# Kernel tuning notes

Hardware: AMD Instinct MI355X
Metric: run time of the kernel (lower is better)

The kernel has to match this reference:

```python
import jax, jax.numpy as jnp
import numpy as np

B, S, D, E, K = 4, 2048, 1024, 8, 2
H = 4 * D


def setup_inputs() -> dict:
    key = jax.random.key(0)
    k0, k1, k2, k3 = jax.random.split(key, 4)
    x = jax.random.normal(k0, (B, S, D), dtype=jnp.float32)
    router_w = jax.random.normal(k1, (E, D), dtype=jnp.float32) * 0.02
    w1 = jax.random.normal(k2, (E, H, D), dtype=jnp.float32) * 0.02  # fc1 weight [out,in]
    w2 = jax.random.normal(k3, (E, D, H), dtype=jnp.float32) * 0.02  # fc2 weight [out,in]
    return {"x": x, "router_w": router_w, "w1": w1, "w2": w2}


def reference(x, router_w, w1, w2):
    b, s, d = x.shape
    e = router_w.shape[0]
    # Router: logits = x @ router_w.T (nn.Linear, bias=False)
    logits = jnp.einsum('bsd,ed->bse', x, router_w)
    probs = jax.nn.softmax(logits, axis=-1)
    topk_vals, topk_idx = jax.lax.top_k(probs, K)  # [b,s,K]

    x_flat = x.reshape(b * s, d)                  # [T, D]
    vals = topk_vals.reshape(b * s, K)            # [T, K]
    idx = topk_idx.reshape(b * s, K)              # [T, K]

    out = jnp.zeros_like(x_flat)
    # Small fixed loop over experts (8); each token gets summed routing weight
    # for this expert over its K slots (equivalent to the torch per-slot scatter-add).
    for eid in range(e):
        w = jnp.sum(jnp.where(idx == eid, vals, jnp.zeros((), x.dtype)), axis=-1)  # [T]
        h = jax.nn.gelu(x_flat @ w1[eid].T, approximate=False)  # [T, H], exact GELU like F.gelu
        y = h @ w2[eid].T                                        # [T, D]
        out = out + w[:, None] * y
    return out.reshape(b, s, d)
```

## Files before the change

kernel.cpp:

```cpp
#include <hip/hip_runtime.h>
#include <hip/hip_bf16.h>
#include <cstdint>

#define TN 8192
#define DN 1024
#define HN 4096
#define EN 8
#define PADMAX 18432

typedef __attribute__((ext_vector_type(8))) short short8;
typedef __attribute__((ext_vector_type(4))) float f32x4;
typedef __attribute__((ext_vector_type(4))) unsigned short ushort4v;

__device__ inline unsigned short f2bf(float f) {
  unsigned u = __builtin_bit_cast(unsigned, f);
  u = u + 0x7fffu + ((u >> 16) & 1u);
  return (unsigned short)(u >> 16);
}
__device__ inline float bf2f(unsigned short u) {
  unsigned v = ((unsigned)u) << 16;
  return __builtin_bit_cast(float, v);
}

__device__ inline float gelu_f(float v) {
  float z2 = 1.5957691216057308f * (v + 0.044715f * v * v * v);
  return v / (1.f + __expf(-z2));
}

__device__ inline void gload_lds16(const void* g, void* l) {
  __builtin_amdgcn_global_load_lds(
      (const __attribute__((address_space(1))) unsigned int*)g,
      (__attribute__((address_space(3))) unsigned int*)l, 16, 0, 0);
}

__global__ __launch_bounds__(256) void cvtw_k(const float* __restrict__ w1,
                                              const float* __restrict__ w2,
                                              unsigned short* __restrict__ d1,
                                              unsigned short* __restrict__ d2) {
  long g = ((long)blockIdx.x * 256 + threadIdx.x) * 8;
  const float* s = blockIdx.y ? w2 : w1;
  unsigned short* d = blockIdx.y ? d2 : d1;
  float4 v0 = *(const float4*)(s + g);
  float4 v1 = *(const float4*)(s + g + 4);
  short8 pk;
  pk[0] = (short)f2bf(v0.x); pk[1] = (short)f2bf(v0.y);
  pk[2] = (short)f2bf(v0.z); pk[3] = (short)f2bf(v0.w);
  pk[4] = (short)f2bf(v1.x); pk[5] = (short)f2bf(v1.y);
  pk[6] = (short)f2bf(v1.z); pk[7] = (short)f2bf(v1.w);
  *(short8*)(d + g) = pk;
}

__global__ __launch_bounds__(256) void router_k(const float* __restrict__ x,
                                                const float* __restrict__ rw,
                                                int* __restrict__ eids,
                                                float* __restrict__ wts) {
  int wid = threadIdx.x >> 6, lane = threadIdx.x & 63;
  int t = blockIdx.x * 4 + wid;
  const float* xr = x + (long)t * DN;
  float a[EN];
#pragma unroll
  for (int e = 0; e < EN; ++e) a[e] = 0.f;
  for (int k = lane; k < DN; k += 64) {
    float xv = xr[k];
#pragma unroll
    for (int e = 0; e < EN; ++e) a[e] += xv * rw[e * DN + k];
  }
#pragma unroll
  for (int off = 32; off > 0; off >>= 1) {
#pragma unroll
    for (int e = 0; e < EN; ++e) a[e] += __shfl_xor(a[e], off);
  }
  if (lane == 0) {
    float mx = a[0];
#pragma unroll
    for (int e = 1; e < EN; ++e) mx = fmaxf(mx, a[e]);
    float p[EN], s = 0.f;
#pragma unroll
    for (int e = 0; e < EN; ++e) { p[e] = __expf(a[e] - mx); s += p[e]; }
    int e0 = 0; float b0 = p[0];
#pragma unroll
    for (int e = 1; e < EN; ++e) if (p[e] > b0) { b0 = p[e]; e0 = e; }
    int e1 = -1; float b1 = -1.f;
#pragma unroll
    for (int e = 0; e < EN; ++e) if (e != e0 && p[e] > b1) { b1 = p[e]; e1 = e; }
    float inv = 1.f / s;
    eids[2 * t] = e0; eids[2 * t + 1] = e1;
    wts[2 * t] = b0 * inv; wts[2 * t + 1] = b1 * inv;
  }
}

__global__ __launch_bounds__(1024) void count_k(const int* __restrict__ eids,
                                                int* __restrict__ poff) {
  __shared__ int hist[16][EN];
  int tid = threadIdx.x, lane = tid & 63, w = tid >> 6;
  int c[EN];
#pragma unroll
  for (int e = 0; e < EN; ++e) c[e] = 0;
  for (int i = tid; i < 2 * TN; i += 1024) {
    int e = eids[i];
#pragma unroll
    for (int j = 0; j < EN; ++j) c[j] += (e == j) ? 1 : 0;
  }
#pragma unroll
  for (int j = 0; j < EN; ++j) {
#pragma unroll
    for (int off = 32; off > 0; off >>= 1) c[j] += __shfl_xor(c[j], off);
  }
  if (lane == 0) {
#pragma unroll
    for (int j = 0; j < EN; ++j) hist[w][j] = c[j];
  }
  __syncthreads();
  if (tid == 0) {
    int o = 0;
    for (int e = 0; e < EN; ++e) {
      int s = 0;
      for (int ww = 0; ww < 16; ++ww) s += hist[ww][e];
      poff[e] = o;
      o += (s + 127) & ~127;
    }
    poff[EN] = o;
  }
}

__global__ __launch_bounds__(256) void scatter_k(const int* __restrict__ eids,
                                                 const float* __restrict__ wts,
                                                 const int* __restrict__ poff,
                                                 int* __restrict__ cursor,
                                                 int* __restrict__ pairTok,
                                                 float* __restrict__ pairW,
                                                 int* __restrict__ slotPos) {
  int t = blockIdx.x * 256 + threadIdx.x;
#pragma unroll
  for (int k = 0; k < 2; ++k) {
    int e = eids[2 * t + k];
    int p = atomicAdd(&cursor[e], 1);
    int pos = poff[e] + p;
    pairTok[pos] = t;
    pairW[pos] = wts[2 * t + k];
    slotPos[2 * t + k] = pos;
  }
}

__global__ __launch_bounds__(256) void gather_k(const float* __restrict__ x,
                                                const int* __restrict__ pairTok,
                                                unsigned short* __restrict__ xg) {
  int p = blockIdx.x * 4 + (threadIdx.x >> 6);
  int lane = threadIdx.x & 63;
  int tok = pairTok[p];
  if (tok < 0) tok = 0;
  const float4* src = (const float4*)(x + (long)tok * DN);
  short8* dst = (short8*)(xg + (long)p * DN);
#pragma unroll
  for (int half = 0; half < 2; ++half) {
    int e8 = half * 64 + lane;
    float4 v0 = src[e8 * 2];
    float4 v1 = src[e8 * 2 + 1];
    short8 pk;
    pk[0] = (short)f2bf(v0.x); pk[1] = (short)f2bf(v0.y);
    pk[2] = (short)f2bf(v0.z); pk[3] = (short)f2bf(v0.w);
    pk[4] = (short)f2bf(v1.x); pk[5] = (short)f2bf(v1.y);
    pk[6] = (short)f2bf(v1.z); pk[7] = (short)f2bf(v1.w);
    dst[e8] = pk;
  }
}

__global__ __launch_bounds__(256) void combine_k(const unsigned short* __restrict__ yb,
                                                 const float* __restrict__ wts,
                                                 const int* __restrict__ slotPos,
                                                 float* __restrict__ out) {
  int t = blockIdx.x;
  int p0 = slotPos[2 * t], p1 = slotPos[2 * t + 1];
  float w0 = wts[2 * t], w1 = wts[2 * t + 1];
  int c = threadIdx.x * 4;
  ushort4v y0 = *(const ushort4v*)(yb + (long)p0 * DN + c);
  ushort4v y1 = *(const ushort4v*)(yb + (long)p1 * DN + c);
  float4 o;
  o.x = w0 * bf2f(y0.x) + w1 * bf2f(y1.x);
  o.y = w0 * bf2f(y0.y) + w1 * bf2f(y1.y);
  o.z = w0 * bf2f(y0.z) + w1 * bf2f(y1.z);
  o.w = w0 * bf2f(y0.w) + w1 * bf2f(y1.w);
  *(float4*)(out + (long)t * DN + c) = o;
}


#define BAR() { asm volatile("" ::: "memory"); __builtin_amdgcn_s_barrier(); \
                asm volatile("" ::: "memory"); }
#define LGKM0() { asm volatile("s_waitcnt lgkmcnt(0)" ::: "memory"); }

#define LDA4(PAR) { const char* _b = smem + (PAR)*16384;                             \
  _Pragma("unroll") for (int m = 0; m < 4; ++m) {                                    \
    int row = waveM*64 + m*16 + (lane & 15); int cb = row * 128;                     \
    a[m][0] = *(const short8*)(_b + cb + (((lane>>4) ^ (row&7)) * 16));              \
    a[m][1] = *(const short8*)(_b + cb + (((4 + (lane>>4)) ^ (row&7)) * 16)); } }

#define LDB2(NH, PAR) { const char* _b = smem + 32768 + (PAR)*16384;                 \
  _Pragma("unroll") for (int n = 0; n < 2; ++n) {                                    \
    int row = waveN*64 + ((NH)*2+n)*16 + (lane & 15); int cb = row * 128;            \
    b[(NH)*2+n][0] = *(const short8*)(_b + cb + (((lane>>4) ^ (row&7)) * 16));       \
    b[(NH)*2+n][1] = *(const short8*)(_b + cb + (((4 + (lane>>4)) ^ (row&7)) * 16)); } }

#define MM16(NH) { __builtin_amdgcn_s_setprio(1);                                    \
  _Pragma("unroll") for (int m = 0; m < 4; ++m)                                      \
    _Pragma("unroll") for (int n = 0; n < 2; ++n) {                                  \
      acc[m][(NH)*2+n] = __builtin_amdgcn_mfma_f32_16x16x32_bf16(                    \
          a[m][0], b[(NH)*2+n][0], acc[m][(NH)*2+n], 0, 0, 0);                       \
      acc[m][(NH)*2+n] = __builtin_amdgcn_mfma_f32_16x16x32_bf16(                    \
          a[m][1], b[(NH)*2+n][1], acc[m][(NH)*2+n], 0, 0, 0); }                     \
  __builtin_amdgcn_s_setprio(0); }

template <int MODE, bool BBF16>
__global__ __launch_bounds__(256, 2) void moe_gemm128_k(
    const unsigned short* __restrict__ Ab, const void* __restrict__ Bsrc,
    void* __restrict__ OutP, const int* __restrict__ pairTok,
    const float* __restrict__ pairW, const int* __restrict__ poff, int chunkStart) {
  constexpr int KD = (MODE == 1) ? DN : HN;
  constexpr int ND = (MODE == 1) ? HN : DN;
  constexpr int SPLIT = (MODE == 3) ? 2 : 1;
  constexpr int KLEN = KD / SPLIT;
  constexpr int NT = KLEN / 64;

  extern __shared__ char smem[];

  int NX = gridDim.x;
  int NXY = NX * gridDim.y;
  int orig = blockIdx.y * NX + blockIdx.x;
  int qq = NXY >> 3, rrm = NXY & 7;
  int xcd = orig & 7, pos = orig >> 3;
  int wg = (xcd < rrm ? xcd * (qq + 1) : rrm * (qq + 1) + (xcd - rrm) * qq) + pos;

  int NYt = NXY / NX;
  const int GH = 8;
  int npg = GH * NX;
  int gid = wg / npg;
  int rem = wg - gid * npg;
  int rowsLeft = NYt - gid * GH;
  int gh = rowsLeft < GH ? rowsLeft : GH;
  int row = gid * GH + rem % gh;
  int col = rem / gh;
  int tileN = col * 128;
  int tileStart = chunkStart + row * 128;

  int Ppad = poff[EN];
  if (tileStart >= Ppad) return;
  int e = 0;
  while (e < EN - 1 && tileStart >= poff[e + 1]) ++e;

  int tid = threadIdx.x;
  int wid = tid >> 6, lane = tid & 63;
  int waveM = wid >> 1, waveN = wid & 1;
  int kbase = (MODE == 3) ? blockIdx.z * KLEN : 0;

  int r0 = tid >> 3;
  const char* aSrc[4];
  const char* bSrc[4];
#pragma unroll
  for (int j = 0; j < 4; ++j) {
    int rw_ = j * 32 + r0;
    int s = (tid & 7) ^ (rw_ & 7);
    long abase = (MODE == 1) ? (long)(tileStart + rw_) * KD
                             : (long)(tileStart - chunkStart + rw_) * KD;
    aSrc[j] = (const char*)(Ab + abase + kbase + s * 8);
    long bb = (long)e * ND * KD + (long)(tileN + rw_) * KD + kbase + s * 8;
    bSrc[j] = (const char*)Bsrc + bb * (BBF16 ? 2 : 4);
  }

  auto stageA = [&](int k0, int par) {
#pragma unroll
    for (int j = 0; j < 4; ++j)
      gload_lds16(aSrc[j] + (long)k0 * 2, smem + par * 16384 + (j * 256 + tid) * 16);
  };
  auto stageB = [&](int k0, int par) {
    if constexpr (BBF16) {
#pragma unroll
      for (int j = 0; j < 4; ++j)
        gload_lds16(bSrc[j] + (long)k0 * 2, smem + 32768 + par * 16384 + (j * 256 + tid) * 16);
    } else {
#pragma unroll
      for (int j = 0; j < 4; ++j) {
        const float4* pf = (const float4*)(bSrc[j] + (long)k0 * 4);
        float4 v0 = pf[0], v1 = pf[1];
        short8 pk;
        pk[0] = (short)f2bf(v0.x); pk[1] = (short)f2bf(v0.y);
        pk[2] = (short)f2bf(v0.z); pk[3] = (short)f2bf(v0.w);
        pk[4] = (short)f2bf(v1.x); pk[5] = (short)f2bf(v1.y);
        pk[6] = (short)f2bf(v1.z); pk[7] = (short)f2bf(v1.w);
        *(short8*)(smem + 32768 + par * 16384 + (j * 256 + tid) * 16) = pk;
      }
    }
  };

  f32x4 acc[4][4];
#pragma unroll
  for (int m = 0; m < 4; ++m)
#pragma unroll
    for (int n = 0; n < 4; ++n) acc[m][n] = (f32x4){0.f, 0.f, 0.f, 0.f};
  short8 a[4][2], b[4][2];

  stageA(0, 0); stageB(0, 0);
  stageA(64, 1); stageB(64, 1);
  if constexpr (BBF16) {
    asm volatile("s_waitcnt vmcnt(8)" ::: "memory");
  } else {
    asm volatile("s_waitcnt vmcnt(0) lgkmcnt(0)" ::: "memory");
  }
  BAR();

  for (int t = 0; t < NT; ++t) {
    int P = t & 1;
    int k2 = (t + 2) * 64;
    LDA4(P); LDB2(0, P);
    BAR(); LGKM0();
    MM16(0);
    BAR();
    LDB2(1, P);
    if (t + 2 < NT) stageA(k2, P);
    BAR(); LGKM0();
    MM16(1);
    if (t + 2 < NT) stageB(k2, P);
    if (BBF16 && t + 2 < NT) {
      asm volatile("s_waitcnt vmcnt(8)" ::: "memory");
    } else {
      asm volatile("s_waitcnt vmcnt(0)" ::: "memory");
    }
    BAR();
  }

  if (MODE == 1) {
    unsigned short* hbp = (unsigned short*)OutP;
    int rl0 = tileStart - chunkStart + waveM * 64;
#pragma unroll
    for (int m = 0; m < 4; ++m) {
#pragma unroll
      for (int r = 0; r < 4; ++r) {
        int rl = rl0 + m * 16 + (lane >> 4) * 4 + r;
#pragma unroll
        for (int n = 0; n < 4; ++n) {
          int coln = tileN + waveN * 64 + n * 16 + (lane & 15);
          hbp[(long)rl * HN + coln] = f2bf(gelu_f(acc[m][n][r]));
        }
      }
    }
  } else if (MODE == 2) {
    unsigned short* ybp = (unsigned short*)OutP;
#pragma unroll
    for (int m = 0; m < 4; ++m) {
#pragma unroll
      for (int r = 0; r < 4; ++r) {
        int p = tileStart + waveM * 64 + m * 16 + (lane >> 4) * 4 + r;
#pragma unroll
        for (int n = 0; n < 4; ++n) {
          int coln = tileN + waveN * 64 + n * 16 + (lane & 15);
          ybp[(long)p * ND + coln] = f2bf(acc[m][n][r]);
        }
      }
    }
  } else {
    float* outF = (float*)OutP;
#pragma unroll
    for (int m = 0; m < 4; ++m) {
#pragma unroll
      for (int r = 0; r < 4; ++r) {
        int p = tileStart + waveM * 64 + m * 16 + (lane >> 4) * 4 + r;
        int tok = pairTok[p];
        if (tok < 0) continue;
        float wv = pairW[p];
#pragma unroll
        for (int n = 0; n < 4; ++n) {
          int coln = tileN + waveN * 64 + n * 16 + (lane & 15);
          atomicAdd(&outF[(long)tok * DN + coln], wv * acc[m][n][r]);
        }
      }
    }
  }
}

extern "C" void kernel_launch(void* const* d_in, const int* in_sizes, int n_in,
                              void* d_out, int out_size, void* d_ws, size_t ws_size,
                              hipStream_t stream) {
  const float* x = (const float*)d_in[0];
  const float* rw = (const float*)d_in[1];
  const float* w1 = (const float*)d_in[2];
  const float* w2 = (const float*)d_in[3];
  char* W = (char*)d_ws;
  size_t off = 0;
  auto alloc = [&](size_t sz) {
    off = (off + 255) & ~(size_t)255;
    size_t r = off; off += sz; return r;
  };
  size_t ctrlO = alloc(256);
  size_t eidsO = alloc((size_t)TN * 2 * 4);
  size_t wtsO  = alloc((size_t)TN * 2 * 4);
  size_t ptokO = alloc((size_t)PADMAX * 4);
  size_t pwO   = alloc((size_t)PADMAX * 4);
  size_t sposO = alloc((size_t)TN * 2 * 4);
  size_t xgO   = alloc((size_t)PADMAX * DN * 2);
  size_t wB = (size_t)EN * HN * DN * 2;
  size_t afterFixed = (off + 255) & ~(size_t)255;
  bool bw = ws_size >= afterFixed + 2 * wB + (size_t)128 * HN * 2 + 4096;
  size_t w1bO = 0, w2bO = 0;
  if (bw) { w1bO = alloc(wB); w2bO = alloc(wB); }
  size_t ybB = (size_t)PADMAX * DN * 2;
  size_t afterW = (off + 255) & ~(size_t)255;
  bool dense = ws_size >= afterW + ybB + (size_t)128 * HN * 2 + 4096;
  size_t ybO = 0;
  if (dense) ybO = alloc(ybB);
  size_t hbase = (off + 255) & ~(size_t)255;
  size_t avail = ws_size > hbase ? ws_size - hbase : (size_t)128 * HN * 2;
  long Cl = (long)(avail / ((size_t)HN * 2));
  if (Cl > PADMAX) Cl = PADMAX;
  Cl &= ~127l;
  if (Cl < 128) Cl = 128;
  int C = (int)Cl;
  size_t hbO = alloc((size_t)C * HN * 2);
  int nCh = (PADMAX + C - 1) / C;

  int* cursor = (int*)(W + ctrlO);
  int* poff = cursor + 8;
  int* eids = (int*)(W + eidsO);
  float* wts = (float*)(W + wtsO);
  int* pairTok = (int*)(W + ptokO);
  float* pairW = (float*)(W + pwO);
  int* slotPos = (int*)(W + sposO);
  unsigned short* xg = (unsigned short*)(W + xgO);
  unsigned short* hb = (unsigned short*)(W + hbO);
  unsigned short* yb = (unsigned short*)(W + ybO);

  hipFuncSetAttribute(reinterpret_cast<const void*>(moe_gemm128_k<1, true>),
                      hipFuncAttributeMaxDynamicSharedMemorySize, 65536);
  hipFuncSetAttribute(reinterpret_cast<const void*>(moe_gemm128_k<2, true>),
                      hipFuncAttributeMaxDynamicSharedMemorySize, 65536);
  hipFuncSetAttribute(reinterpret_cast<const void*>(moe_gemm128_k<3, true>),
                      hipFuncAttributeMaxDynamicSharedMemorySize, 65536);
  hipFuncSetAttribute(reinterpret_cast<const void*>(moe_gemm128_k<1, false>),
                      hipFuncAttributeMaxDynamicSharedMemorySize, 65536);
  hipFuncSetAttribute(reinterpret_cast<const void*>(moe_gemm128_k<2, false>),
                      hipFuncAttributeMaxDynamicSharedMemorySize, 65536);
  hipFuncSetAttribute(reinterpret_cast<const void*>(moe_gemm128_k<3, false>),
                      hipFuncAttributeMaxDynamicSharedMemorySize, 65536);

  hipMemsetAsync(W + ctrlO, 0, 256, stream);
  hipMemsetAsync(W + ptokO, 0xFF, (size_t)PADMAX * 4, stream);
  if (!dense) hipMemsetAsync(d_out, 0, (size_t)TN * DN * 4, stream);

  if (bw) {
    cvtw_k<<<dim3((int)((long)EN * HN * DN / (8 * 256)), 2), 256, 0, stream>>>(
        w1, w2, (unsigned short*)(W + w1bO), (unsigned short*)(W + w2bO));
  }
  router_k<<<TN / 4, 256, 0, stream>>>(x, rw, eids, wts);
  count_k<<<1, 1024, 0, stream>>>(eids, poff);
  scatter_k<<<TN / 256, 256, 0, stream>>>(eids, wts, poff, cursor, pairTok, pairW, slotPos);
  gather_k<<<PADMAX / 4, 256, 0, stream>>>(x, pairTok, xg);

  int Ctiles = C / 128;
  for (int c = 0; c < nCh; ++c) {
    int cs = c * C;
    if (bw) {
      moe_gemm128_k<1, true><<<dim3(HN / 128, Ctiles, 1), 256, 65536, stream>>>(
          xg, W + w1bO, hb, pairTok, pairW, poff, cs);
      if (dense) {
        moe_gemm128_k<2, true><<<dim3(DN / 128, Ctiles, 1), 256, 65536, stream>>>(
            hb, W + w2bO, yb, pairTok, pairW, poff, cs);
      } else {
        moe_gemm128_k<3, true><<<dim3(DN / 128, Ctiles, 2), 256, 65536, stream>>>(
            hb, W + w2bO, d_out, pairTok, pairW, poff, cs);
      }
    } else {
      moe_gemm128_k<1, false><<<dim3(HN / 128, Ctiles, 1), 256, 65536, stream>>>(
          xg, w1, hb, pairTok, pairW, poff, cs);
      if (dense) {
        moe_gemm128_k<2, false><<<dim3(DN / 128, Ctiles, 1), 256, 65536, stream>>>(
            hb, w2, yb, pairTok, pairW, poff, cs);
      } else {
        moe_gemm128_k<3, false><<<dim3(DN / 128, Ctiles, 2), 256, 65536, stream>>>(
            hb, w2, d_out, pairTok, pairW, poff, cs);
      }
    }
  }
  if (dense) {
    combine_k<<<TN, 256, 0, stream>>>(yb, wts, slotPos, (float*)d_out);
  }
}
```

Baseline: 559.8 us.

## Fuse router with bf16 conversions and gather rows inside the first GEMM

The router, the weight conversion and a new dense x-to-bf16 conversion now run in a single prep kernel, with extra blocks doing a grid-stride conversion loop. The separate gather kernel that copied and converted x rows into a padded expert-sorted buffer is removed. Instead, the first GEMM reads A rows indirectly through pairTok from the dense bf16 copy of x. This saves a kernel launch, a padded buffer write and a re-read, at the cost of non-contiguous A row loads in the GEMM.

```diff
diff --git a/kernel.cpp b/kernel.cpp
--- a/kernel.cpp
+++ b/kernel.cpp
@@ -33,59 +33,70 @@
       (__attribute__((address_space(3))) unsigned int*)l, 16, 0, 0);
 }
 
-__global__ __launch_bounds__(256) void cvtw_k(const float* __restrict__ w1,
+__global__ __launch_bounds__(256) void prep_k(const float* __restrict__ x,
+                                              const float* __restrict__ rw,
+                                              const float* __restrict__ w1,
                                               const float* __restrict__ w2,
-                                              unsigned short* __restrict__ d1,
-                                              unsigned short* __restrict__ d2) {
-  long g = ((long)blockIdx.x * 256 + threadIdx.x) * 8;
-  const float* s = blockIdx.y ? w2 : w1;
-  unsigned short* d = blockIdx.y ? d2 : d1;
-  float4 v0 = *(const float4*)(s + g);
-  float4 v1 = *(const float4*)(s + g + 4);
-  short8 pk;
-  pk[0] = (short)f2bf(v0.x); pk[1] = (short)f2bf(v0.y);
-  pk[2] = (short)f2bf(v0.z); pk[3] = (short)f2bf(v0.w);
-  pk[4] = (short)f2bf(v1.x); pk[5] = (short)f2bf(v1.y);
-  pk[6] = (short)f2bf(v1.z); pk[7] = (short)f2bf(v1.w);
-  *(short8*)(d + g) = pk;
-}
-
-__global__ __launch_bounds__(256) void router_k(const float* __restrict__ x,
-                                                const float* __restrict__ rw,
-                                                int* __restrict__ eids,
-                                                float* __restrict__ wts) {
-  int wid = threadIdx.x >> 6, lane = threadIdx.x & 63;
-  int t = blockIdx.x * 4 + wid;
-  const float* xr = x + (long)t * DN;
-  float a[EN];
-#pragma unroll
-  for (int e = 0; e < EN; ++e) a[e] = 0.f;
-  for (int k = lane; k < DN; k += 64) {
-    float xv = xr[k];
-#pragma unroll
-    for (int e = 0; e < EN; ++e) a[e] += xv * rw[e * DN + k];
-  }
-#pragma unroll
-  for (int off = 32; off > 0; off >>= 1) {
-#pragma unroll
-    for (int e = 0; e < EN; ++e) a[e] += __shfl_xor(a[e], off);
-  }
-  if (lane == 0) {
-    float mx = a[0];
-#pragma unroll
-    for (int e = 1; e < EN; ++e) mx = fmaxf(mx, a[e]);
-    float p[EN], s = 0.f;
-#pragma unroll
-    for (int e = 0; e < EN; ++e) { p[e] = __expf(a[e] - mx); s += p[e]; }
-    int e0 = 0; float b0 = p[0];
-#pragma unroll
-    for (int e = 1; e < EN; ++e) if (p[e] > b0) { b0 = p[e]; e0 = e; }
-    int e1 = -1; float b1 = -1.f;
-#pragma unroll
-    for (int e = 0; e < EN; ++e) if (e != e0 && p[e] > b1) { b1 = p[e]; e1 = e; }
-    float inv = 1.f / s;
-    eids[2 * t] = e0; eids[2 * t + 1] = e1;
-    wts[2 * t] = b0 * inv; wts[2 * t + 1] = b1 * inv;
+                                              unsigned short* __restrict__ xb,
+                                              unsigned short* __restrict__ w1b,
+                                              unsigned short* __restrict__ w2b,
+                                              int* __restrict__ eids,
+                                              float* __restrict__ wts,
+                                              int nCvtBlk, long nGroups) {
+  if (blockIdx.x < TN / 4) {
+    int wid = threadIdx.x >> 6, lane = threadIdx.x & 63;
+    int t = blockIdx.x * 4 + wid;
+    const float* xr = x + (long)t * DN;
+    float a[EN];
+#pragma unroll
+    for (int e = 0; e < EN; ++e) a[e] = 0.f;
+    for (int k = lane; k < DN; k += 64) {
+      float xv = xr[k];
+#pragma unroll
+      for (int e = 0; e < EN; ++e) a[e] += xv * rw[e * DN + k];
+    }
+#pragma unroll
+    for (int off = 32; off > 0; off >>= 1) {
+#pragma unroll
+      for (int e = 0; e < EN; ++e) a[e] += __shfl_xor(a[e], off);
+    }
+    if (lane == 0) {
+      float mx = a[0];
+#pragma unroll
+      for (int e = 1; e < EN; ++e) mx = fmaxf(mx, a[e]);
+      float p[EN], s = 0.f;
+#pragma unroll
+      for (int e = 0; e < EN; ++e) { p[e] = __expf(a[e] - mx); s += p[e]; }
+      int e0 = 0; float b0 = p[0];
+#pragma unroll
+      for (int e = 1; e < EN; ++e) if (p[e] > b0) { b0 = p[e]; e0 = e; }
+      int e1 = -1; float b1 = -1.f;
+#pragma unroll
+      for (int e = 0; e < EN; ++e) if (e != e0 && p[e] > b1) { b1 = p[e]; e1 = e; }
+      float inv = 1.f / s;
+      eids[2 * t] = e0; eids[2 * t + 1] = e1;
+      wts[2 * t] = b0 * inv; wts[2 * t + 1] = b1 * inv;
+    }
+  } else {
+    const long GX = (long)TN * DN / 8;
+    const long GW = (long)EN * HN * DN / 8;
+    long g = (long)(blockIdx.x - TN / 4) * 256 + threadIdx.x;
+    long stride = (long)nCvtBlk * 256;
+    for (; g < nGroups; g += stride) {
+      const float* s; unsigned short* d; long j;
+      if (g < GX) { s = x; d = xb; j = g; }
+      else if (g < GX + GW) { s = w1; d = w1b; j = g - GX; }
+      else { s = w2; d = w2b; j = g - GX - GW; }
+      long e8 = j * 8;
+      float4 v0 = *(const float4*)(s + e8);
+      float4 v1 = *(const float4*)(s + e8 + 4);
+      short8 pk;
+      pk[0] = (short)f2bf(v0.x); pk[1] = (short)f2bf(v0.y);
+      pk[2] = (short)f2bf(v0.z); pk[3] = (short)f2bf(v0.w);
+      pk[4] = (short)f2bf(v1.x); pk[5] = (short)f2bf(v1.y);
+      pk[6] = (short)f2bf(v1.z); pk[7] = (short)f2bf(v1.w);
+      *(short8*)(d + e8) = pk;
+    }
   }
 }
 
@@ -139,29 +150,6 @@
     pairTok[pos] = t;
     pairW[pos] = wts[2 * t + k];
     slotPos[2 * t + k] = pos;
-  }
-}
-
-__global__ __launch_bounds__(256) void gather_k(const float* __restrict__ x,
-                                                const int* __restrict__ pairTok,
-                                                unsigned short* __restrict__ xg) {
-  int p = blockIdx.x * 4 + (threadIdx.x >> 6);
-  int lane = threadIdx.x & 63;
-  int tok = pairTok[p];
-  if (tok < 0) tok = 0;
-  const float4* src = (const float4*)(x + (long)tok * DN);
-  short8* dst = (short8*)(xg + (long)p * DN);
-#pragma unroll
-  for (int half = 0; half < 2; ++half) {
-    int e8 = half * 64 + lane;
-    float4 v0 = src[e8 * 2];
-    float4 v1 = src[e8 * 2 + 1];
-    short8 pk;
-    pk[0] = (short)f2bf(v0.x); pk[1] = (short)f2bf(v0.y);
-    pk[2] = (short)f2bf(v0.z); pk[3] = (short)f2bf(v0.w);
-    pk[4] = (short)f2bf(v1.x); pk[5] = (short)f2bf(v1.y);
-    pk[6] = (short)f2bf(v1.z); pk[7] = (short)f2bf(v1.w);
-    dst[e8] = pk;
   }
 }
 
@@ -258,8 +246,14 @@
   for (int j = 0; j < 4; ++j) {
     int rw_ = j * 32 + r0;
     int s = (tid & 7) ^ (rw_ & 7);
-    long abase = (MODE == 1) ? (long)(tileStart + rw_) * KD
-                             : (long)(tileStart - chunkStart + rw_) * KD;
+    long abase;
+    if (MODE == 1) {
+      int tok = pairTok[tileStart + rw_];
+      if (tok < 0) tok = 0;
+      abase = (long)tok * KD;
+    } else {
+      abase = (long)(tileStart - chunkStart + rw_) * KD;
+    }
     aSrc[j] = (const char*)(Ab + abase + kbase + s * 8);
     long bb = (long)e * ND * KD + (long)(tileN + rw_) * KD + kbase + s * 8;
     bSrc[j] = (const char*)Bsrc + bb * (BBF16 ? 2 : 4);
@@ -394,7 +388,7 @@
   size_t ptokO = alloc((size_t)PADMAX * 4);
   size_t pwO   = alloc((size_t)PADMAX * 4);
   size_t sposO = alloc((size_t)TN * 2 * 4);
-  size_t xgO   = alloc((size_t)PADMAX * DN * 2);
+  size_t xbO   = alloc((size_t)TN * DN * 2);
   size_t wB = (size_t)EN * HN * DN * 2;
   size_t afterFixed = (off + 255) & ~(size_t)255;
   bool bw = ws_size >= afterFixed + 2 * wB + (size_t)128 * HN * 2 + 4096;
@@ -422,7 +416,7 @@
   int* pairTok = (int*)(W + ptokO);
   float* pairW = (float*)(W + pwO);
   int* slotPos = (int*)(W + sposO);
-  unsigned short* xg = (unsigned short*)(W + xgO);
+  unsigned short* xb = (unsigned short*)(W + xbO);
   unsigned short* hb = (unsigned short*)(W + hbO);
   unsigned short* yb = (unsigned short*)(W + ybO);
 
@@ -443,21 +437,24 @@
   hipMemsetAsync(W + ptokO, 0xFF, (size_t)PADMAX * 4, stream);
   if (!dense) hipMemsetAsync(d_out, 0, (size_t)TN * DN * 4, stream);
 
-  if (bw) {
-    cvtw_k<<<dim3((int)((long)EN * HN * DN / (8 * 256)), 2), 256, 0, stream>>>(
-        w1, w2, (unsigned short*)(W + w1bO), (unsigned short*)(W + w2bO));
-  }
-  router_k<<<TN / 4, 256, 0, stream>>>(x, rw, eids, wts);
+  const int nCvtBlk = 4096;
+  const long GX = (long)TN * DN / 8;
+  const long GW = (long)EN * HN * DN / 8;
+  long nGroups = GX + (bw ? 2 * GW : 0);
+  prep_k<<<TN / 4 + nCvtBlk, 256, 0, stream>>>(
+      x, rw, w1, w2, xb,
+      bw ? (unsigned short*)(W + w1bO) : nullptr,
+      bw ? (unsigned short*)(W + w2bO) : nullptr,
+      eids, wts, nCvtBlk, nGroups);
   count_k<<<1, 1024, 0, stream>>>(eids, poff);
   scatter_k<<<TN / 256, 256, 0, stream>>>(eids, wts, poff, cursor, pairTok, pairW, slotPos);
-  gather_k<<<PADMAX / 4, 256, 0, stream>>>(x, pairTok, xg);
 
   int Ctiles = C / 128;
   for (int c = 0; c < nCh; ++c) {
     int cs = c * C;
     if (bw) {
       moe_gemm128_k<1, true><<<dim3(HN / 128, Ctiles, 1), 256, 65536, stream>>>(
-          xg, W + w1bO, hb, pairTok, pairW, poff, cs);
+          xb, W + w1bO, hb, pairTok, pairW, poff, cs);
       if (dense) {
         moe_gemm128_k<2, true><<<dim3(DN / 128, Ctiles, 1), 256, 65536, stream>>>(
             hb, W + w2bO, yb, pairTok, pairW, poff, cs);
@@ -467,7 +464,7 @@
       }
     } else {
       moe_gemm128_k<1, false><<<dim3(HN / 128, Ctiles, 1), 256, 65536, stream>>>(
-          xg, w1, hb, pairTok, pairW, poff, cs);
+          xb, w1, hb, pairTok, pairW, poff, cs);
       if (dense) {
         moe_gemm128_k<2, false><<<dim3(DN / 128, Ctiles, 1), 256, 65536, stream>>>(
             hb, w2, yb, pairTok, pairW, poff, cs);
```

Result: no change. 554.4 us (-1.0%).
